# Kernel tuning notes

Measured on AMD Instinct MI355X. Metric: run time of the kernel, lower is better.

Reference implementation:

```python
import jax, jax.numpy as jnp
import numpy as np

H = 512          # hidden_dim
D = 128          # input_dim
L = 8            # output_dim == NUMLABELS
T = 64           # encoder time steps per frame-feature sequence
W = 240          # WINDOWWIDTH (encoder batch dim, one element per frame)
CTX = W // 4     # 60 attention positions
NSTEPS = W // 8


def _lstm(x, Wih, Whh, bih, bhh):
    """PyTorch-convention LSTM (gate order i,f,g,o). x: (T,B,Din) -> (outputs (T,B,H), final h (B,H))."""
    B = x.shape[1]
    Hh = Whh.shape[1]
    xp = jnp.einsum('tbd,gd->tbg', x, Wih) + bih + bhh  # fold both biases
    def step(carry, g):
        h, c = carry
        g = g + h @ Whh.T
        i, f, gg, o = jnp.split(g, 4, axis=-1)
        c = jax.nn.sigmoid(f) * c + jax.nn.sigmoid(i) * jnp.tanh(gg)
        h = jax.nn.sigmoid(o) * jnp.tanh(c)
        return (h, c), h
    z = jnp.zeros((B, Hh), x.dtype)
    (hT, _), hs = jax.lax.scan(step, (z, z), xp)
    return hs, hT


def _forward(data, enc_Wih, enc_Whh, enc_bih, enc_bhh,
             p1f_Wih, p1f_Whh, p1f_bih, p1f_bhh, p1b_Wih, p1b_Whh, p1b_bih, p1b_bhh,
             p2f_Wih, p2f_Whh, p2f_bih, p2f_bhh, p2b_Wih, p2b_Whh, p2b_bih, p2b_bhh,
             attn_W, attn_b, comb_W, comb_b,
             gru_Wih, gru_Whh, gru_bih, gru_bhh, out_W, out_b):
    # --- encoder: per-frame LSTM over T steps, keep final hidden per frame ---
    _, h_enc = _lstm(data, enc_Wih, enc_Whh, enc_bih, enc_bhh)          # (W, H)
    # --- pyramidal bi-LSTM 1: pairs of frames ---
    x1 = h_enc.reshape(W // 2, 1, 2 * H)
    f1, _ = _lstm(x1, p1f_Wih, p1f_Whh, p1f_bih, p1f_bhh)
    b1, _ = _lstm(x1[::-1], p1b_Wih, p1b_Whh, p1b_bih, p1b_bhh)
    # --- pyramidal bi-LSTM 2 ---
    x2 = jnp.concatenate([f1, b1[::-1]], axis=-1).reshape(W // 4, 1, 4 * H)
    f2, h2T = _lstm(x2, p2f_Wih, p2f_Whh, p2f_bih, p2f_bhh)
    b2, _ = _lstm(x2[::-1], p2b_Wih, p2b_Whh, p2b_bih, p2b_bhh)
    ctx = jnp.concatenate([f2, b2[::-1]], axis=-1).reshape(CTX, 2 * H)  # (60, 2H)
    h = h2T[0]                                   # forward-direction final hidden, (H,)
    inp0 = jnp.zeros((L,), data.dtype).at[L - 1].set(1.0)  # one_hot(NOLABEL)

    def dec_step(carry, _):
        inp, h = carry
        aw = jax.nn.softmax(attn_W @ jnp.concatenate([inp, h]) + attn_b)    # (60,)
        applied = aw @ ctx                                                   # (2H,)
        o = jax.nn.relu(comb_W @ jnp.concatenate([inp, applied]) + comb_b)  # (H,)
        # PyTorch GRU cell (gate order r,z,n)
        gi = gru_Wih @ o + gru_bih
        gh = gru_Whh @ h + gru_bhh
        ir, iz, inn = jnp.split(gi, 3)
        hr, hz, hn = jnp.split(gh, 3)
        r = jax.nn.sigmoid(ir + hr)
        z = jax.nn.sigmoid(iz + hz)
        n = jnp.tanh(inn + r * hn)
        h_new = (1.0 - z) * n + z * h
        logp = jax.nn.log_softmax(out_W @ h_new + out_b)                     # (L,)
        return (logp, h_new), logp  # prediction feeds back as next input (y=None path)

    _, outputs = jax.lax.scan(dec_step, (inp0, h), None, length=NSTEPS)
    return outputs  # (30, L)


def setup_inputs() -> dict:
    key = jax.random.key(0)
    ks = iter(jax.random.split(key, 64))
    def mk(*shape):
        return (jax.random.normal(next(ks), shape) * 0.05).astype(jnp.float32)
    d = {"data": jax.random.normal(next(ks), (T, W, D), dtype=jnp.float32)}
    d.update(enc_Wih=mk(4 * H, D), enc_Whh=mk(4 * H, H), enc_bih=mk(4 * H), enc_bhh=mk(4 * H))
    for p, din in (("p1f", 2 * H), ("p1b", 2 * H), ("p2f", 4 * H), ("p2b", 4 * H)):
        d[p + "_Wih"] = mk(4 * H, din)
        d[p + "_Whh"] = mk(4 * H, H)
        d[p + "_bih"] = mk(4 * H)
        d[p + "_bhh"] = mk(4 * H)
    d.update(attn_W=mk(CTX, H + L), attn_b=mk(CTX), comb_W=mk(H, 2 * H + L), comb_b=mk(H),
             gru_Wih=mk(3 * H, H), gru_Whh=mk(3 * H, H), gru_bih=mk(3 * H), gru_bhh=mk(3 * H),
             out_W=mk(L, H), out_b=mk(L))
    return d


def reference(data, enc_Wih, enc_Whh, enc_bih, enc_bhh,
              p1f_Wih, p1f_Whh, p1f_bih, p1f_bhh, p1b_Wih, p1b_Whh, p1b_bih, p1b_bhh,
              p2f_Wih, p2f_Whh, p2f_bih, p2f_bhh, p2b_Wih, p2b_Whh, p2b_bih, p2b_bhh,
              attn_W, attn_b, comb_W, comb_b,
              gru_Wih, gru_Whh, gru_bih, gru_bhh, out_W, out_b):
    return _forward(data, enc_Wih, enc_Whh, enc_bih, enc_bhh,
                    p1f_Wih, p1f_Whh, p1f_bih, p1f_bhh, p1b_Wih, p1b_Whh, p1b_bih, p1b_bhh,
                    p2f_Wih, p2f_Whh, p2f_bih, p2f_bhh, p2b_Wih, p2b_Whh, p2b_bih, p2b_bhh,
                    attn_W, attn_b, comb_W, comb_b,
                    gru_Wih, gru_Whh, gru_bih, gru_bhh, out_W, out_b)
```

## Files before the change

kernel.cpp:

```cpp
#include <hip/hip_runtime.h>
#include <math.h>


typedef __attribute__((ext_vector_type(8))) short short8;
typedef __attribute__((ext_vector_type(4))) float floatx4;
typedef unsigned long long ull;

__device__ __forceinline__ float sigf(float x) { return 1.f / (1.f + __expf(-x)); }
__device__ __forceinline__ float tanh_f(float x) {
    float e = __expf(2.f * x);
    return 1.f - 2.f / (e + 1.f);
}
__device__ __forceinline__ unsigned short f2b(float x) {
    unsigned u = __float_as_uint(x);
    unsigned r = (u + 0x7FFFu + ((u >> 16) & 1u)) >> 16;
    return (unsigned short)r;
}

__device__ __forceinline__ float gld(const float* p) {
    return __hip_atomic_load(p, __ATOMIC_RELAXED, __HIP_MEMORY_SCOPE_AGENT);
}
__device__ __forceinline__ void gst(float* p, float v) {
    __hip_atomic_store(p, v, __ATOMIC_RELAXED, __HIP_MEMORY_SCOPE_AGENT);
}
__device__ __forceinline__ ull gldll(const ull* p) {
    return __hip_atomic_load(p, __ATOMIC_RELAXED, __HIP_MEMORY_SCOPE_AGENT);
}
__device__ __forceinline__ void gstll(ull* p, ull v) {
    __hip_atomic_store(p, v, __ATOMIC_RELAXED, __HIP_MEMORY_SCOPE_AGENT);
}
__device__ __forceinline__ ull packfe(float d, int ep) {
    return ((ull)(unsigned)ep << 32) | (ull)__float_as_uint(d);
}
__device__ __forceinline__ float lowf(ull v) { return __uint_as_float((unsigned)v); }

__global__ void init_k(float* __restrict__ ws) {
    for (int i = blockIdx.x * blockDim.x + threadIdx.x; i < 256000; i += gridDim.x * blockDim.x)
        ws[i] = 0.f;
}

__global__ void __launch_bounds__(256, 1) enc_all(
    const float* __restrict__ data,
    const float* __restrict__ Wih, const float* __restrict__ Whh,
    const float* __restrict__ bih, const float* __restrict__ bhh,
    ull* __restrict__ hbufF,
    float* __restrict__ henc)
{
    __shared__ short act2[20 * 64 * 8];
    __shared__ float gw[4][640];
    __shared__ float cs[512];
    __shared__ short hw[4][16][8];
    __shared__ float biasL[4][4][8];

    const int tid = threadIdx.x;
    const int fg = blockIdx.x >> 4, ds = blockIdx.x & 15;
    const int w = tid >> 6, lane = tid & 63;
    const int n = lane & 15, q = lane >> 4;

    short8 bfrag[2][20];
#pragma unroll
    for (int nt = 0; nt < 2; ++nt) {
        int rr = nt * 16 + n;
        int g = rr >> 3, dp = rr & 7;
        int grow = g * 512 + ds * 32 + w * 8 + dp;
#pragma unroll
        for (int kt = 0; kt < 20; ++kt) {
            int k0 = kt * 32 + q * 8;
            const float* src = (k0 < 512) ? (Whh + (size_t)grow * 512 + k0)
                                          : (Wih + (size_t)grow * 128 + (k0 - 512));
            float4 lo = *(const float4*)src;
            float4 hi = *(const float4*)(src + 4);
            short8 bf;
            bf[0] = (short)f2b(lo.x); bf[1] = (short)f2b(lo.y);
            bf[2] = (short)f2b(lo.z); bf[3] = (short)f2b(lo.w);
            bf[4] = (short)f2b(hi.x); bf[5] = (short)f2b(hi.y);
            bf[6] = (short)f2b(hi.z); bf[7] = (short)f2b(hi.w);
            bfrag[nt][kt] = bf;
        }
    }
    if (tid < 128) {
        int w2 = tid >> 5, rr = tid & 31;
        int g = rr >> 3, dp = rr & 7;
        int grow = g * 512 + ds * 32 + w2 * 8 + dp;
        biasL[w2][g][dp] = bih[grow] + bhh[grow];
    }
    for (int i = tid; i < 512; i += 256) cs[i] = 0.f;
    __syncthreads();

    unsigned* a2u = (unsigned*)act2;

    for (int t = 0; t < 64; ++t) {
        const int kt2 = tid >> 6, l2 = tid & 63, f2v = l2 & 15, q2 = l2 >> 4;
        const float* xs = data + ((size_t)t * 240 + fg * 16 + f2v) * 128 + kt2 * 32 + q2 * 8;
        float4 lo = *(const float4*)xs;
        float4 hi = *(const float4*)(xs + 4);

        {
            const ull* hsrc = hbufF + (size_t)((t & 1) * 15 + fg) * 4096;
            ull v[16];
            for (;;) {
                bool ok = true;
#pragma unroll
                for (int k2 = 0; k2 < 16; ++k2) {
                    v[k2] = gldll(hsrc + tid + 256 * k2);
                    ok &= ((int)(v[k2] >> 32) == t);
                }
                if (ok) break;
                __builtin_amdgcn_s_sleep(1);
            }
#pragma unroll
            for (int k2 = 0; k2 < 16; ++k2)
                a2u[tid + 256 * k2] = (unsigned)v[k2];
        }
        {
            short8 xp;
            xp[0] = (short)f2b(lo.x); xp[1] = (short)f2b(lo.y);
            xp[2] = (short)f2b(lo.z); xp[3] = (short)f2b(lo.w);
            xp[4] = (short)f2b(hi.x); xp[5] = (short)f2b(hi.y);
            xp[6] = (short)f2b(hi.z); xp[7] = (short)f2b(hi.w);
            *(short8*)&act2[((16 + kt2) * 64 + l2) * 8] = xp;
        }
        __syncthreads();

        floatx4 acc0 = {0.f, 0.f, 0.f, 0.f};
        floatx4 acc1 = {0.f, 0.f, 0.f, 0.f};
#pragma unroll
        for (int kt = 0; kt < 20; ++kt) {
            short8 a = *(short8*)&act2[(kt * 64 + lane) * 8];
            acc0 = __builtin_amdgcn_mfma_f32_16x16x32_bf16(a, bfrag[0][kt], acc0, 0, 0, 0);
            acc1 = __builtin_amdgcn_mfma_f32_16x16x32_bf16(a, bfrag[1][kt], acc1, 0, 0, 0);
        }
        *(floatx4*)&gw[w][(0 * 16 + n) * 20 + 4 * q] = acc0;
        *(floatx4*)&gw[w][(1 * 16 + n) * 20 + 4 * q] = acc1;

        int nb = (t + 1) & 1;
#pragma unroll
        for (int it = 0; it < 2; ++it) {
            int f = lane & 15, dp = q + 4 * it;
            float gi = gw[w][(0 * 8 + dp) * 20 + f] + biasL[w][0][dp];
            float gf = gw[w][(1 * 8 + dp) * 20 + f] + biasL[w][1][dp];
            float gg = gw[w][(2 * 8 + dp) * 20 + f] + biasL[w][2][dp];
            float go = gw[w][(3 * 8 + dp) * 20 + f] + biasL[w][3][dp];
            int ci = f * 32 + w * 8 + dp;
            float cc = cs[ci];
            float cn = sigf(gf) * cc + sigf(gi) * tanh_f(gg);
            float hn = sigf(go) * tanh_f(cn);
            cs[ci] = cn;
            hw[w][f][dp] = (short)f2b(hn);
            if (t == 63)
                gst(&henc[(size_t)(fg * 16 + f) * 512 + ds * 32 + w * 8 + dp], hn);
        }
        if (lane < 16) {
            const unsigned* hwu = (const unsigned*)&hw[w][lane][0];
            ull* dst = hbufF + (size_t)(nb * 15 + fg) * 4096 + (ds * 64 + w * 16 + lane) * 4;
            const ull ep = ((ull)(unsigned)(t + 1)) << 32;
#pragma unroll
            for (int r = 0; r < 4; ++r)
                gstll(dst + r, ep | (ull)hwu[r]);
        }
        __syncthreads();
    }
}

__global__ void __launch_bounds__(256) gemm_xp2(
    const float* __restrict__ A, int M, int K, int halfgrid,
    const float* __restrict__ WvF, const float* __restrict__ baF,
    const float* __restrict__ bbF, float* __restrict__ CF,
    const float* __restrict__ WvB, const float* __restrict__ baB,
    const float* __restrict__ bbB, float* __restrict__ CB)
{
    __shared__ float At[16][66];
    __shared__ float Wt[128][66];
    const int tid = threadIdx.x;
    int bgl = blockIdx.x;
    const int rev = (bgl >= halfgrid) ? 1 : 0;
    if (rev) bgl -= halfgrid;
    const float* Wv = rev ? WvB : WvF;
    const float* ba = rev ? baB : baF;
    const float* bb = rev ? bbB : bbF;
    float* C        = rev ? CB : CF;

    const int nt = bgl & 15, mt = bgl >> 4;
    const int rp = tid >> 2, fq = tid & 3;
    const int lr0 = 2 * rp, lr1 = lr0 + 1;
    const int n0 = nt * 128 + lr0, n1 = n0 + 1;

    float acc0[4], acc1[4];
    {
        float b0 = ba[n0] + bb[n0], b1 = ba[n1] + bb[n1];
#pragma unroll
        for (int j = 0; j < 4; ++j) { acc0[j] = b0; acc1[j] = b1; }
    }

    for (int kt = 0; kt < K; kt += 64) {
        {
            int f = tid >> 4, c4 = tid & 15;
            int m = mt * 16 + f;
            float4 v = make_float4(0.f, 0.f, 0.f, 0.f);
            if (m < M) {
                int ar = rev ? (M - 1 - m) : m;
                v = ((const float4*)(A + (size_t)ar * K + kt))[c4];
            }
            At[f][c4 * 4 + 0] = v.x; At[f][c4 * 4 + 1] = v.y;
            At[f][c4 * 4 + 2] = v.z; At[f][c4 * 4 + 3] = v.w;
        }
        for (int i = tid; i < 2048; i += 256) {
            int lr = i >> 4, c4 = i & 15;
            float4 v = ((const float4*)(Wv + (size_t)(nt * 128 + lr) * K + kt))[c4];
            Wt[lr][c4 * 4 + 0] = v.x; Wt[lr][c4 * 4 + 1] = v.y;
            Wt[lr][c4 * 4 + 2] = v.z; Wt[lr][c4 * 4 + 3] = v.w;
        }
        __syncthreads();
        const float2* w0p = (const float2*)(&Wt[lr0][0]);
        const float2* w1p = (const float2*)(&Wt[lr1][0]);
#pragma unroll 8
        for (int kh = 0; kh < 32; ++kh) {
            float2 w0 = w0p[kh], w1 = w1p[kh];
#pragma unroll
            for (int j = 0; j < 4; ++j) {
                float2 av = ((const float2*)(&At[4 * fq + j][0]))[kh];
                acc0[j] += w0.x * av.x + w0.y * av.y;
                acc1[j] += w1.x * av.x + w1.y * av.y;
            }
        }
        __syncthreads();
    }
#pragma unroll
    for (int j = 0; j < 4; ++j) {
        int m = mt * 16 + 4 * fq + j;
        if (m < M) {
            C[(size_t)m * 2048 + n0] = acc0[j];
            C[(size_t)m * 2048 + n1] = acc1[j];
        }
    }
}

__global__ void __launch_bounds__(256, 1) pyr_rec(
    const float* __restrict__ xpF, const float* __restrict__ xpB,
    const float* __restrict__ WhhF, const float* __restrict__ WhhB,
    ull* __restrict__ hp,
    float* __restrict__ outF, float* __restrict__ outB,
    int steps)
{
    const int tid = threadIdx.x;
    const int dir = blockIdx.x >> 6, blk = blockIdx.x & 63;
    const float* xp  = dir ? xpB : xpF;
    const float* Whh = dir ? WhhB : WhhF;
    float* outp = dir ? outB : outF;
    ull* hpd = hp + (size_t)dir * 1024;

    __shared__ __align__(16) float hcur[512];
    __shared__ float red[32][9];
    __shared__ float gv[32];

    const int lr = tid & 31, seg = tid >> 5;
    const int grow = (lr >> 3) * 512 + blk * 8 + (lr & 7);
    float4 wl4[16];
#pragma unroll
    for (int j = 0; j < 16; ++j)
        wl4[j] = *(const float4*)&Whh[(size_t)grow * 512 + 4 * seg + 32 * j];

    const int growx = (tid >> 3) * 512 + blk * 8 + (tid & 7);
    float creg = 0.f;
    __syncthreads();

    for (int t = 0; t < steps; ++t) {
        float xg = 0.f;
        if (tid < 32) xg = xp[(size_t)t * 2048 + growx];
        {
            const ull* base = hpd + (size_t)(t & 1) * 512;
            ull v0 = gldll(base + tid), v1 = gldll(base + tid + 256);
            while (((int)(v0 >> 32) != t) | ((int)(v1 >> 32) != t)) {
                __builtin_amdgcn_s_sleep(1);
                v0 = gldll(base + tid);
                v1 = gldll(base + tid + 256);
            }
            hcur[tid]       = lowf(v0);
            hcur[tid + 256] = lowf(v1);
        }
        __syncthreads();

        float a = 0.f;
#pragma unroll
        for (int j = 0; j < 16; ++j) {
            float4 w = wl4[j];
            float4 h4 = *(const float4*)&hcur[4 * seg + 32 * j];
            a += w.x*h4.x + w.y*h4.y + w.z*h4.z + w.w*h4.w;
        }
        red[lr][seg] = a;
        __syncthreads();

        if (tid < 32) {
            float g = xg;
#pragma unroll
            for (int s2 = 0; s2 < 8; ++s2) g += red[tid][s2];
            gv[tid] = g;
        }
        __syncthreads();
        if (tid < 8) {
            float i_ = sigf(gv[tid]), f_ = sigf(gv[8 + tid]);
            float g_ = tanh_f(gv[16 + tid]), o_ = sigf(gv[24 + tid]);
            creg = f_ * creg + i_ * g_;
            float hn = o_ * tanh_f(creg);
            int d = blk * 8 + tid;
            gstll(&hpd[((t + 1) & 1) * 512 + d], packfe(hn, t + 1));
            int row = dir ? (steps - 1 - t) : t;
            outp[(size_t)row * 512 + d] = hn;
        }
        __syncthreads();
    }
}

__global__ void x2_assemble(const float* __restrict__ f1, const float* __restrict__ b1o,
                            float* __restrict__ x2)
{
    int j = blockIdx.x;
    for (int k = threadIdx.x; k < 2048; k += 256) {
        int q = k >> 9, r = k & 511;
        const float* src = (q & 1) ? b1o : f1;
        int row = 2 * j + (q >> 1);
        x2[(size_t)j * 2048 + k] = src[(size_t)row * 512 + r];
    }
}

__global__ void ctx_k(const float* __restrict__ f2, const float* __restrict__ b2o,
                      float* __restrict__ ctx, ull* __restrict__ hdec_p)
{
    int j = blockIdx.x;
    for (int k = threadIdx.x; k < 1024; k += 256)
        ctx[(size_t)j * 1024 + k] = (k < 512) ? f2[(size_t)j * 512 + k]
                                              : b2o[(size_t)j * 512 + k - 512];
    if (j == 0) {
        for (int i = threadIdx.x; i < 512; i += 256)
            hdec_p[i] = packfe(f2[59 * 512 + i], 0);
    }
}

__global__ void __launch_bounds__(256) precomp_M(
    const float* __restrict__ comb_W,
    const float* __restrict__ ctx,
    float* __restrict__ Mg)
{
    __shared__ float cw[8 * 1024];
    const int tid = threadIdx.x, d0 = blockIdx.x * 8;
    for (int i = tid; i < 2048; i += 256) {
        int r = i >> 8, c4 = i & 255;
        float4 v = *(const float4*)&comb_W[(size_t)(d0 + r) * 1032 + 8 + 4 * c4];
        *(float4*)&cw[r * 1024 + 4 * c4] = v;
    }
    __syncthreads();
    for (int o = tid; o < 480; o += 256) {
        int dl = o / 60, j = o % 60;
        const float4* cp = (const float4*)&cw[dl * 1024];
        const float4* xp = (const float4*)(ctx + (size_t)j * 1024);
        float a = 0.f;
#pragma unroll 4
        for (int k = 0; k < 256; ++k) {
            float4 w = cp[k], x = xp[k];
            a += w.x * x.x + w.y * x.y + w.z * x.z + w.w * x.w;
        }
        Mg[(size_t)(d0 + dl) * 60 + j] = a;
    }
}

__global__ void __launch_bounds__(256, 1) dec_k(
    const float* __restrict__ attn_W, const float* __restrict__ attn_b,
    const float* __restrict__ comb_W, const float* __restrict__ comb_b,
    const float* __restrict__ gWih, const float* __restrict__ gWhh,
    const float* __restrict__ gbih, const float* __restrict__ gbhh,
    const float* __restrict__ outW, const float* __restrict__ outb,
    const float* __restrict__ Mg,
    ull* __restrict__ hdec_p,
    float* __restrict__ dout)
{
    const int tid = threadIdx.x, bid = blockIdx.x;
    const int dbase = bid * 8;

    __shared__ float M2[512][70];
    __shared__ __align__(16) float hx[528];
    __shared__ __align__(16) float xl[512];
    __shared__ __align__(8) float awx[68];
    __shared__ float redA[64][5];
    __shared__ float redGH[32][9];
    __shared__ float redG[32][9];
    __shared__ float redO[8][33];
    __shared__ float biasg[24], biasi[24];
    __shared__ float cbL[512];
    __shared__ float attnbL[64];

    float4 wa4[33], wo4[4], wg4[16], wi4[16];
    const int rz = tid >> 2, sz = tid & 3;
    const int ro = tid >> 5, so = tid & 31;
    const int rg = tid >> 3, sg = tid & 7;

    {
        int rr = (rz < 60) ? rz : 59;
#pragma unroll
        for (int i = 0; i < 32; ++i)
            wa4[i] = *(const float4*)&attn_W[(size_t)rr * 520 + 4 * sz + 16 * i];
        float* wap = (float*)&wa4[32];
#pragma unroll
        for (int r = 0; r < 4; ++r) {
            int k = 4 * sz + 512 + r;
            wap[r] = (k < 520) ? attn_W[(size_t)rr * 520 + k] : 0.f;
        }
    }
#pragma unroll
    for (int i = 0; i < 4; ++i)
        wo4[i] = *(const float4*)&outW[(size_t)ro * 512 + 4 * so + 128 * i];
    {
        int rr = (rg < 24) ? rg : 23;
        int grow = (rr >> 3) * 512 + dbase + (rr & 7);
#pragma unroll
        for (int j = 0; j < 16; ++j) {
            wg4[j] = *(const float4*)&gWhh[(size_t)grow * 512 + 4 * sg + 32 * j];
            wi4[j] = *(const float4*)&gWih[(size_t)grow * 512 + 4 * sg + 32 * j];
        }
    }
    if (tid < 24) {
        int g2 = (tid >> 3) * 512 + dbase + (tid & 7);
        biasg[tid] = gbhh[g2];
        biasi[tid] = gbih[g2];
    }
    for (int i = tid; i < 512; i += 256) cbL[i] = comb_b[i];
    if (tid < 64) attnbL[tid] = (tid < 60) ? attn_b[tid] : 0.f;
    if (tid < 8) hx[520 + tid] = 0.f;
    for (int i = tid; i < 512 * 15; i += 256) {
        int r = i / 15, c4 = i % 15;
        float4 v = *(const float4*)&Mg[(size_t)r * 60 + 4 * c4];
        M2[r][4 * c4 + 0] = v.x; M2[r][4 * c4 + 1] = v.y;
        M2[r][4 * c4 + 2] = v.z; M2[r][4 * c4 + 3] = v.w;
    }
    for (int i = tid; i < 512 * 2; i += 256) {
        int r = i >> 1, h4 = i & 1;
        float4 v = *(const float4*)&comb_W[(size_t)r * 1032 + 4 * h4];
        M2[r][60 + 4 * h4 + 0] = v.x; M2[r][60 + 4 * h4 + 1] = v.y;
        M2[r][60 + 4 * h4 + 2] = v.z; M2[r][60 + 4 * h4 + 3] = v.w;
    }
    __syncthreads();

    for (int s = 0; s < 30; ++s) {
        {
            const ull* hs = hdec_p + (size_t)(s & 1) * 512;
            ull v0 = gldll(hs + tid), v1 = gldll(hs + tid + 256);
            while (((int)(v0 >> 32) != s) | ((int)(v1 >> 32) != s)) {
                __builtin_amdgcn_s_sleep(1);
                v0 = gldll(hs + tid);
                v1 = gldll(hs + tid + 256);
            }
            hx[8 + tid]       = lowf(v0);
            hx[8 + tid + 256] = lowf(v1);
        }
        __syncthreads();

        if (s > 0) {
            float a = 0.f;
#pragma unroll
            for (int i = 0; i < 4; ++i) {
                float4 w = wo4[i];
                float4 h4 = *(const float4*)&hx[8 + 4 * so + 128 * i];
                a += w.x*h4.x + w.y*h4.y + w.z*h4.z + w.w*h4.w;
            }
            redO[ro][so] = a;
        }
        {
            float a = 0.f;
#pragma unroll
            for (int j = 0; j < 16; ++j) {
                float4 w = wg4[j];
                float4 h4 = *(const float4*)&hx[8 + 4 * sg + 32 * j];
                a += w.x*h4.x + w.y*h4.y + w.z*h4.z + w.w*h4.w;
            }
            redGH[rg][sg] = a;
        }
        __syncthreads();

        if (tid < 8) {
            float v;
            if (s > 0) {
                float a = outb[tid];
#pragma unroll
                for (int g2 = 0; g2 < 32; ++g2) a += redO[tid][g2];
                float m = a;
                m = fmaxf(m, __shfl_xor(m, 1));
                m = fmaxf(m, __shfl_xor(m, 2));
                m = fmaxf(m, __shfl_xor(m, 4));
                float e = __expf(a - m);
                float ss2 = e;
                ss2 += __shfl_xor(ss2, 1);
                ss2 += __shfl_xor(ss2, 2);
                ss2 += __shfl_xor(ss2, 4);
                v = a - m - __logf(ss2);
                if (bid == 0) dout[(s - 1) * 8 + tid] = v;
            } else {
                v = (tid == 7) ? 1.f : 0.f;
            }
            hx[tid] = v;
            awx[60 + tid] = v;
        }
        __syncthreads();

        {
            float a = 0.f;
#pragma unroll
            for (int i = 0; i < 33; ++i) {
                float4 w = wa4[i];
                float4 x4 = *(const float4*)&hx[4 * sz + 16 * i];
                a += w.x*x4.x + w.y*x4.y + w.z*x4.z + w.w*x4.w;
            }
            redA[rz][sz] = a;
        }
        __syncthreads();

        if (tid < 64) {
            float z = -1e30f;
            if (tid < 60)
                z = attnbL[tid] + redA[tid][0] + redA[tid][1] + redA[tid][2] + redA[tid][3];
            float m = z;
#pragma unroll
            for (int off = 32; off; off >>= 1) m = fmaxf(m, __shfl_xor(m, off));
            float e = (tid < 60) ? __expf(z - m) : 0.f;
            float ss2 = e;
#pragma unroll
            for (int off = 32; off; off >>= 1) ss2 += __shfl_xor(ss2, off);
            if (tid < 60) awx[tid] = e / ss2;
        }
        __syncthreads();

#pragma unroll
        for (int half = 0; half < 2; ++half) {
            int c = tid + half * 256;
            float a = cbL[c];
            const float2* mrow = (const float2*)&M2[c][0];
            const float2* xv = (const float2*)&awx[0];
#pragma unroll
            for (int jj = 0; jj < 34; ++jj) {
                float2 mm = mrow[jj], xx = xv[jj];
                a += mm.x * xx.x + mm.y * xx.y;
            }
            xl[c] = fmaxf(a, 0.f);
        }
        __syncthreads();

        {
            float a = 0.f;
#pragma unroll
            for (int j = 0; j < 16; ++j) {
                float4 w = wi4[j];
                float4 o4 = *(const float4*)&xl[4 * sg + 32 * j];
                a += w.x*o4.x + w.y*o4.y + w.z*o4.z + w.w*o4.w;
            }
            redG[rg][sg] = a;
        }
        __syncthreads();

        if (tid < 8) {
            float gh0 = biasg[tid], gh1 = biasg[8 + tid], gh2 = biasg[16 + tid];
            float gi0 = biasi[tid], gi1 = biasi[8 + tid], gi2 = biasi[16 + tid];
#pragma unroll
            for (int g2 = 0; g2 < 8; ++g2) {
                gh0 += redGH[tid][g2]; gh1 += redGH[8 + tid][g2]; gh2 += redGH[16 + tid][g2];
                gi0 += redG[tid][g2];  gi1 += redG[8 + tid][g2];  gi2 += redG[16 + tid][g2];
            }
            float r_ = sigf(gi0 + gh0);
            float z_ = sigf(gi1 + gh1);
            float n_ = tanh_f(gi2 + r_ * gh2);
            float hnew = (1.f - z_) * n_ + z_ * hx[8 + dbase + tid];
            gstll(&hdec_p[(size_t)((s + 1) & 1) * 512 + dbase + tid], packfe(hnew, s + 1));
        }
        __syncthreads();
    }

    if (bid == 0) {
        {
            const ull* hs = hdec_p + (size_t)(30 & 1) * 512;
            ull v0 = gldll(hs + tid), v1 = gldll(hs + tid + 256);
            while (((int)(v0 >> 32) != 30) | ((int)(v1 >> 32) != 30)) {
                __builtin_amdgcn_s_sleep(1);
                v0 = gldll(hs + tid);
                v1 = gldll(hs + tid + 256);
            }
            hx[8 + tid]       = lowf(v0);
            hx[8 + tid + 256] = lowf(v1);
        }
        __syncthreads();
        {
            float a = 0.f;
#pragma unroll
            for (int i = 0; i < 4; ++i) {
                float4 w = wo4[i];
                float4 h4 = *(const float4*)&hx[8 + 4 * so + 128 * i];
                a += w.x*h4.x + w.y*h4.y + w.z*h4.z + w.w*h4.w;
            }
            redO[ro][so] = a;
        }
        __syncthreads();
        if (tid < 8) {
            float a = outb[tid];
#pragma unroll
            for (int g2 = 0; g2 < 32; ++g2) a += redO[tid][g2];
            float m = a;
            m = fmaxf(m, __shfl_xor(m, 1));
            m = fmaxf(m, __shfl_xor(m, 2));
            m = fmaxf(m, __shfl_xor(m, 4));
            float e = __expf(a - m);
            float ss2 = e;
            ss2 += __shfl_xor(ss2, 1);
            ss2 += __shfl_xor(ss2, 2);
            ss2 += __shfl_xor(ss2, 4);
            dout[29 * 8 + tid] = a - m - __logf(ss2);
        }
    }
}

extern "C" void kernel_launch(void* const* d_in, const int* in_sizes, int n_in,
                              void* d_out, int out_size, void* d_ws, size_t ws_size,
                              hipStream_t stream) {
    (void)in_sizes; (void)n_in; (void)out_size; (void)ws_size;
    const float* data    = (const float*)d_in[0];
    const float* enc_Wih = (const float*)d_in[1];
    const float* enc_Whh = (const float*)d_in[2];
    const float* enc_bih = (const float*)d_in[3];
    const float* enc_bhh = (const float*)d_in[4];
    const float* p1f_Wih = (const float*)d_in[5];
    const float* p1f_Whh = (const float*)d_in[6];
    const float* p1f_bih = (const float*)d_in[7];
    const float* p1f_bhh = (const float*)d_in[8];
    const float* p1b_Wih = (const float*)d_in[9];
    const float* p1b_Whh = (const float*)d_in[10];
    const float* p1b_bih = (const float*)d_in[11];
    const float* p1b_bhh = (const float*)d_in[12];
    const float* p2f_Wih = (const float*)d_in[13];
    const float* p2f_Whh = (const float*)d_in[14];
    const float* p2f_bih = (const float*)d_in[15];
    const float* p2f_bhh = (const float*)d_in[16];
    const float* p2b_Wih = (const float*)d_in[17];
    const float* p2b_Whh = (const float*)d_in[18];
    const float* p2b_bih = (const float*)d_in[19];
    const float* p2b_bhh = (const float*)d_in[20];
    const float* attn_W  = (const float*)d_in[21];
    const float* attn_b  = (const float*)d_in[22];
    const float* comb_W  = (const float*)d_in[23];
    const float* comb_b  = (const float*)d_in[24];
    const float* gru_Wih = (const float*)d_in[25];
    const float* gru_Whh = (const float*)d_in[26];
    const float* gru_bih = (const float*)d_in[27];
    const float* gru_bhh = (const float*)d_in[28];
    const float* out_W   = (const float*)d_in[29];
    const float* out_b   = (const float*)d_in[30];

    float* ws = (float*)d_ws;
    ull* hbufF   = (ull*)ws;
    ull* hp1     = (ull*)(ws + 245760);
    ull* hp2     = (ull*)(ws + 249856);
    ull* hdec_p  = (ull*)(ws + 253952);
    float* henc  = ws + 256000;
    float* xp1f  = ws + 378880;
    float* xp1b  = ws + 624640;
    float* f1    = ws + 870400;
    float* b1o   = ws + 931840;
    float* x2    = ws + 993280;
    float* xp2f  = ws + 1116160;
    float* xp2b  = ws + 1239040;
    float* f2    = ws + 1361920;
    float* b2o   = ws + 1392640;
    float* ctxb  = ws + 1423360;
    float* Mg    = ws + 1484800;

    init_k<<<256, 256, 0, stream>>>(ws);

    enc_all<<<240, 256, 0, stream>>>(data, enc_Wih, enc_Whh, enc_bih, enc_bhh,
                                     hbufF, henc);
    gemm_xp2<<<256, 256, 0, stream>>>(henc, 120, 1024, 128,
                                      p1f_Wih, p1f_bih, p1f_bhh, xp1f,
                                      p1b_Wih, p1b_bih, p1b_bhh, xp1b);
    pyr_rec<<<128, 256, 0, stream>>>(xp1f, xp1b, p1f_Whh, p1b_Whh, hp1, f1, b1o, 120);
    x2_assemble<<<60, 256, 0, stream>>>(f1, b1o, x2);
    gemm_xp2<<<128, 256, 0, stream>>>(x2, 60, 2048, 64,
                                      p2f_Wih, p2f_bih, p2f_bhh, xp2f,
                                      p2b_Wih, p2b_bih, p2b_bhh, xp2b);
    pyr_rec<<<128, 256, 0, stream>>>(xp2f, xp2b, p2f_Whh, p2b_Whh, hp2, f2, b2o, 60);
    ctx_k<<<60, 256, 0, stream>>>(f2, b2o, ctxb, hdec_p);
    precomp_M<<<64, 256, 0, stream>>>(comb_W, ctxb, Mg);
    dec_k<<<64, 256, 0, stream>>>(attn_W, attn_b, comb_W, comb_b,
                                  gru_Wih, gru_Whh, gru_bih, gru_bhh,
                                  out_W, out_b, Mg, hdec_p,
                                  (float*)d_out);
}
```

Baseline: 1.318 ms.

## Restructure decoder kernel to 512 threads with shuffle reductions and fewer barriers

The decoder kernel moves from 256 to 512 threads per block and swaps its shared-memory partial-sum arrays for wave shuffle reductions. The attention logits are split into a hidden-state part, computed in parallel with the GRU hidden and output projections, and an 8-wide label part folded into the softmax wave. This removes two block barriers per decode step and shortens the serial chain on the recurrent critical path. The cost is more threads per block and different register pressure, and the decoder is only part of the total pipeline time.

```diff
diff --git a/kernel.cpp b/kernel.cpp
--- a/kernel.cpp
+++ b/kernel.cpp
@@ -363,7 +363,7 @@
     }
 }
 
-__global__ void __launch_bounds__(256, 1) dec_k(
+__global__ void __launch_bounds__(512, 1) dec_k(
     const float* __restrict__ attn_W, const float* __restrict__ attn_b,
     const float* __restrict__ comb_W, const float* __restrict__ comb_b,
     const float* __restrict__ gWih, const float* __restrict__ gWhh,
@@ -374,64 +374,67 @@
     float* __restrict__ dout)
 {
     const int tid = threadIdx.x, bid = blockIdx.x;
+    const int lane = tid & 63, wv = tid >> 6;
     const int dbase = bid * 8;
 
     __shared__ float M2[512][70];
-    __shared__ __align__(16) float hx[528];
+    __shared__ __align__(16) float hL[520];
     __shared__ __align__(16) float xl[512];
-    __shared__ __align__(8) float awx[68];
-    __shared__ float redA[64][5];
-    __shared__ float redGH[32][9];
-    __shared__ float redG[32][9];
-    __shared__ float redO[8][33];
+    __shared__ __align__(16) float awx[68];
+    __shared__ float zd[8], zh[64];
+    __shared__ float ghl[24], gil[24];
     __shared__ float biasg[24], biasi[24];
     __shared__ float cbL[512];
-    __shared__ float attnbL[64];
-
-    float4 wa4[33], wo4[4], wg4[16], wi4[16];
-    const int rz = tid >> 2, sz = tid & 3;
-    const int ro = tid >> 5, so = tid & 31;
-    const int rg = tid >> 3, sg = tid & 7;
-
+    __shared__ float attnbL[64], outbL[8];
+
+    const int rg = tid >> 4, sg = tid & 15;
+    const int rz = tid >> 3, szz = tid & 7;
+
+    float4 wo2[2];
+    float4 wg8[8], wi8[8];
+    float4 wzh[16];
+    float4 wip[2];
+    {
+        const float* wp = outW + (size_t)wv * 512 + lane * 8;
+        wo2[0] = *(const float4*)wp;
+        wo2[1] = *(const float4*)(wp + 4);
+    }
+    {
+        int rr = (rg < 24) ? rg : 23;
+        size_t grow = (size_t)((rr >> 3) * 512 + dbase + (rr & 7)) * 512 + sg * 32;
+#pragma unroll
+        for (int i = 0; i < 8; ++i) {
+            wg8[i] = *(const float4*)&gWhh[grow + 4 * i];
+            wi8[i] = *(const float4*)&gWih[grow + 4 * i];
+        }
+    }
     {
         int rr = (rz < 60) ? rz : 59;
-#pragma unroll
-        for (int i = 0; i < 32; ++i)
-            wa4[i] = *(const float4*)&attn_W[(size_t)rr * 520 + 4 * sz + 16 * i];
-        float* wap = (float*)&wa4[32];
-#pragma unroll
-        for (int r = 0; r < 4; ++r) {
-            int k = 4 * sz + 512 + r;
-            wap[r] = (k < 520) ? attn_W[(size_t)rr * 520 + k] : 0.f;
-        }
-    }
-#pragma unroll
-    for (int i = 0; i < 4; ++i)
-        wo4[i] = *(const float4*)&outW[(size_t)ro * 512 + 4 * so + 128 * i];
+        size_t base = (size_t)rr * 520 + 8 + szz * 64;
+#pragma unroll
+        for (int i = 0; i < 16; ++i)
+            wzh[i] = *(const float4*)&attn_W[base + 4 * i];
+    }
     {
-        int rr = (rg < 24) ? rg : 23;
-        int grow = (rr >> 3) * 512 + dbase + (rr & 7);
-#pragma unroll
-        for (int j = 0; j < 16; ++j) {
-            wg4[j] = *(const float4*)&gWhh[(size_t)grow * 512 + 4 * sg + 32 * j];
-            wi4[j] = *(const float4*)&gWih[(size_t)grow * 512 + 4 * sg + 32 * j];
-        }
+        int rr = (tid < 60) ? tid : 59;
+        wip[0] = *(const float4*)&attn_W[(size_t)rr * 520 + 0];
+        wip[1] = *(const float4*)&attn_W[(size_t)rr * 520 + 4];
     }
     if (tid < 24) {
         int g2 = (tid >> 3) * 512 + dbase + (tid & 7);
         biasg[tid] = gbhh[g2];
         biasi[tid] = gbih[g2];
     }
-    for (int i = tid; i < 512; i += 256) cbL[i] = comb_b[i];
+    if (tid < 512) cbL[tid] = comb_b[tid];
     if (tid < 64) attnbL[tid] = (tid < 60) ? attn_b[tid] : 0.f;
-    if (tid < 8) hx[520 + tid] = 0.f;
-    for (int i = tid; i < 512 * 15; i += 256) {
+    if (tid < 8) outbL[tid] = outb[tid];
+    for (int i = tid; i < 512 * 15; i += 512) {
         int r = i / 15, c4 = i % 15;
         float4 v = *(const float4*)&Mg[(size_t)r * 60 + 4 * c4];
         M2[r][4 * c4 + 0] = v.x; M2[r][4 * c4 + 1] = v.y;
         M2[r][4 * c4 + 2] = v.z; M2[r][4 * c4 + 3] = v.w;
     }
-    for (int i = tid; i < 512 * 2; i += 256) {
+    for (int i = tid; i < 512 * 2; i += 512) {
         int r = i >> 1, h4 = i & 1;
         float4 v = *(const float4*)&comb_W[(size_t)r * 1032 + 4 * h4];
         M2[r][60 + 4 * h4 + 0] = v.x; M2[r][60 + 4 * h4 + 1] = v.y;
@@ -442,130 +445,131 @@
     for (int s = 0; s < 30; ++s) {
         {
             const ull* hs = hdec_p + (size_t)(s & 1) * 512;
-            ull v0 = gldll(hs + tid), v1 = gldll(hs + tid + 256);
-            while (((int)(v0 >> 32) != s) | ((int)(v1 >> 32) != s)) {
+            ull v0 = gldll(hs + tid);
+            while ((int)(v0 >> 32) != s) {
                 __builtin_amdgcn_s_sleep(1);
                 v0 = gldll(hs + tid);
-                v1 = gldll(hs + tid + 256);
-            }
-            hx[8 + tid]       = lowf(v0);
-            hx[8 + tid + 256] = lowf(v1);
-        }
-        __syncthreads();
-
-        if (s > 0) {
+            }
+            hL[tid] = lowf(v0);
+        }
+        __syncthreads();
+
+        {
             float a = 0.f;
-#pragma unroll
-            for (int i = 0; i < 4; ++i) {
-                float4 w = wo4[i];
-                float4 h4 = *(const float4*)&hx[8 + 4 * so + 128 * i];
+            const float4* h4p = (const float4*)&hL[lane * 8];
+            float4 h0 = h4p[0], h1 = h4p[1];
+            a += wo2[0].x*h0.x + wo2[0].y*h0.y + wo2[0].z*h0.z + wo2[0].w*h0.w;
+            a += wo2[1].x*h1.x + wo2[1].y*h1.y + wo2[1].z*h1.z + wo2[1].w*h1.w;
+#pragma unroll
+            for (int off = 32; off; off >>= 1) a += __shfl_xor(a, off);
+            if (lane == 0) zd[wv] = a;
+        }
+        {
+            float a = 0.f;
+            const float* hb = &hL[sg * 32];
+#pragma unroll
+            for (int i = 0; i < 8; ++i) {
+                float4 w = wg8[i];
+                float4 h4 = *(const float4*)&hb[4 * i];
                 a += w.x*h4.x + w.y*h4.y + w.z*h4.z + w.w*h4.w;
             }
-            redO[ro][so] = a;
+            a += __shfl_xor(a, 1); a += __shfl_xor(a, 2);
+            a += __shfl_xor(a, 4); a += __shfl_xor(a, 8);
+            if (sg == 0 && rg < 24) ghl[rg] = a;
         }
         {
             float a = 0.f;
-#pragma unroll
-            for (int j = 0; j < 16; ++j) {
-                float4 w = wg4[j];
-                float4 h4 = *(const float4*)&hx[8 + 4 * sg + 32 * j];
+            const float* hb = &hL[szz * 64];
+#pragma unroll
+            for (int i = 0; i < 16; ++i) {
+                float4 w = wzh[i];
+                float4 h4 = *(const float4*)&hb[4 * i];
                 a += w.x*h4.x + w.y*h4.y + w.z*h4.z + w.w*h4.w;
             }
-            redGH[rg][sg] = a;
-        }
-        __syncthreads();
-
-        if (tid < 8) {
-            float v;
-            if (s > 0) {
-                float a = outb[tid];
-#pragma unroll
-                for (int g2 = 0; g2 < 32; ++g2) a += redO[tid][g2];
-                float m = a;
-                m = fmaxf(m, __shfl_xor(m, 1));
-                m = fmaxf(m, __shfl_xor(m, 2));
-                m = fmaxf(m, __shfl_xor(m, 4));
-                float e = __expf(a - m);
-                float ss2 = e;
-                ss2 += __shfl_xor(ss2, 1);
-                ss2 += __shfl_xor(ss2, 2);
-                ss2 += __shfl_xor(ss2, 4);
-                v = a - m - __logf(ss2);
-                if (bid == 0) dout[(s - 1) * 8 + tid] = v;
-            } else {
-                v = (tid == 7) ? 1.f : 0.f;
-            }
-            hx[tid] = v;
-            awx[60 + tid] = v;
-        }
-        __syncthreads();
-
-        {
-            float a = 0.f;
-#pragma unroll
-            for (int i = 0; i < 33; ++i) {
-                float4 w = wa4[i];
-                float4 x4 = *(const float4*)&hx[4 * sz + 16 * i];
-                a += w.x*x4.x + w.y*x4.y + w.z*x4.z + w.w*x4.w;
-            }
-            redA[rz][sz] = a;
-        }
-        __syncthreads();
-
-        if (tid < 64) {
+            a += __shfl_xor(a, 1); a += __shfl_xor(a, 2); a += __shfl_xor(a, 4);
+            if (szz == 0 && rz < 60) zh[rz] = a;
+        }
+        __syncthreads();
+
+        if (wv == 0) {
+            if (lane < 8) {
+                float v;
+                if (s > 0) {
+                    float a = zd[lane] + outbL[lane];
+                    float m = a;
+                    m = fmaxf(m, __shfl_xor(m, 1));
+                    m = fmaxf(m, __shfl_xor(m, 2));
+                    m = fmaxf(m, __shfl_xor(m, 4));
+                    float e = __expf(a - m);
+                    float ss2 = e;
+                    ss2 += __shfl_xor(ss2, 1);
+                    ss2 += __shfl_xor(ss2, 2);
+                    ss2 += __shfl_xor(ss2, 4);
+                    v = a - m - __logf(ss2);
+                    if (bid == 0) dout[(s - 1) * 8 + lane] = v;
+                } else {
+                    v = (lane == 7) ? 1.f : 0.f;
+                }
+                awx[60 + lane] = v;
+            }
             float z = -1e30f;
-            if (tid < 60)
-                z = attnbL[tid] + redA[tid][0] + redA[tid][1] + redA[tid][2] + redA[tid][3];
+            if (lane < 60) {
+                z = zh[lane] + attnbL[lane]
+                  + wip[0].x * awx[60] + wip[0].y * awx[61]
+                  + wip[0].z * awx[62] + wip[0].w * awx[63]
+                  + wip[1].x * awx[64] + wip[1].y * awx[65]
+                  + wip[1].z * awx[66] + wip[1].w * awx[67];
+            }
             float m = z;
 #pragma unroll
             for (int off = 32; off; off >>= 1) m = fmaxf(m, __shfl_xor(m, off));
-            float e = (tid < 60) ? __expf(z - m) : 0.f;
+            float e = (lane < 60) ? __expf(z - m) : 0.f;
             float ss2 = e;
 #pragma unroll
             for (int off = 32; off; off >>= 1) ss2 += __shfl_xor(ss2, off);
-            if (tid < 60) awx[tid] = e / ss2;
-        }
-        __syncthreads();
-
-#pragma unroll
-        for (int half = 0; half < 2; ++half) {
-            int c = tid + half * 256;
-            float a = cbL[c];
-            const float2* mrow = (const float2*)&M2[c][0];
+            if (lane < 60) awx[lane] = e / ss2;
+        }
+        __syncthreads();
+
+        {
+            float a = cbL[tid];
+            const float2* mrow = (const float2*)&M2[tid][0];
             const float2* xv = (const float2*)&awx[0];
 #pragma unroll
             for (int jj = 0; jj < 34; ++jj) {
                 float2 mm = mrow[jj], xx = xv[jj];
                 a += mm.x * xx.x + mm.y * xx.y;
             }
-            xl[c] = fmaxf(a, 0.f);
+            xl[tid] = fmaxf(a, 0.f);
         }
         __syncthreads();
 
         {
             float a = 0.f;
-#pragma unroll
-            for (int j = 0; j < 16; ++j) {
-                float4 w = wi4[j];
-                float4 o4 = *(const float4*)&xl[4 * sg + 32 * j];
+            const float* ob = &xl[sg * 32];
+#pragma unroll
+            for (int i = 0; i < 8; ++i) {
+                float4 w = wi8[i];
+                float4 o4 = *(const float4*)&ob[4 * i];
                 a += w.x*o4.x + w.y*o4.y + w.z*o4.z + w.w*o4.w;
             }
-            redG[rg][sg] = a;
+            a += __shfl_xor(a, 1); a += __shfl_xor(a, 2);
+            a += __shfl_xor(a, 4); a += __shfl_xor(a, 8);
+            if (sg == 0 && rg < 24) gil[rg] = a;
         }
         __syncthreads();
 
         if (tid < 8) {
-            float gh0 = biasg[tid], gh1 = biasg[8 + tid], gh2 = biasg[16 + tid];
-            float gi0 = biasi[tid], gi1 = biasi[8 + tid], gi2 = biasi[16 + tid];
-#pragma unroll
-            for (int g2 = 0; g2 < 8; ++g2) {
-                gh0 += redGH[tid][g2]; gh1 += redGH[8 + tid][g2]; gh2 += redGH[16 + tid][g2];
-                gi0 += redG[tid][g2];  gi1 += redG[8 + tid][g2];  gi2 += redG[16 + tid][g2];
-            }
+            float gh0 = biasg[tid] + ghl[tid];
+            float gh1 = biasg[8 + tid] + ghl[8 + tid];
+            float gh2 = biasg[16 + tid] + ghl[16 + tid];
+            float gi0 = biasi[tid] + gil[tid];
+            float gi1 = biasi[8 + tid] + gil[8 + tid];
+            float gi2 = biasi[16 + tid] + gil[16 + tid];
             float r_ = sigf(gi0 + gh0);
             float z_ = sigf(gi1 + gh1);
             float n_ = tanh_f(gi2 + r_ * gh2);
-            float hnew = (1.f - z_) * n_ + z_ * hx[8 + dbase + tid];
+            float hnew = (1.f - z_) * n_ + z_ * hL[dbase + tid];
             gstll(&hdec_p[(size_t)((s + 1) & 1) * 512 + dbase + tid], packfe(hnew, s + 1));
         }
         __syncthreads();
@@ -574,31 +578,27 @@
     if (bid == 0) {
         {
             const ull* hs = hdec_p + (size_t)(30 & 1) * 512;
-            ull v0 = gldll(hs + tid), v1 = gldll(hs + tid + 256);
-            while (((int)(v0 >> 32) != 30) | ((int)(v1 >> 32) != 30)) {
+            ull v0 = gldll(hs + tid);
+            while ((int)(v0 >> 32) != 30) {
                 __builtin_amdgcn_s_sleep(1);
                 v0 = gldll(hs + tid);
-                v1 = gldll(hs + tid + 256);
-            }
-            hx[8 + tid]       = lowf(v0);
-            hx[8 + tid + 256] = lowf(v1);
+            }
+            hL[tid] = lowf(v0);
         }
         __syncthreads();
         {
             float a = 0.f;
-#pragma unroll
-            for (int i = 0; i < 4; ++i) {
-                float4 w = wo4[i];
-                float4 h4 = *(const float4*)&hx[8 + 4 * so + 128 * i];
-                a += w.x*h4.x + w.y*h4.y + w.z*h4.z + w.w*h4.w;
-            }
-            redO[ro][so] = a;
+            const float4* h4p = (const float4*)&hL[lane * 8];
+            float4 h0 = h4p[0], h1 = h4p[1];
+            a += wo2[0].x*h0.x + wo2[0].y*h0.y + wo2[0].z*h0.z + wo2[0].w*h0.w;
+            a += wo2[1].x*h1.x + wo2[1].y*h1.y + wo2[1].z*h1.z + wo2[1].w*h1.w;
+#pragma unroll
+            for (int off = 32; off; off >>= 1) a += __shfl_xor(a, off);
+            if (lane == 0) zd[wv] = a;
         }
         __syncthreads();
         if (tid < 8) {
-            float a = outb[tid];
-#pragma unroll
-            for (int g2 = 0; g2 < 32; ++g2) a += redO[tid][g2];
+            float a = zd[tid] + outbL[tid];
             float m = a;
             m = fmaxf(m, __shfl_xor(m, 1));
             m = fmaxf(m, __shfl_xor(m, 2));
@@ -682,7 +682,7 @@
     pyr_rec<<<128, 256, 0, stream>>>(xp2f, xp2b, p2f_Whh, p2b_Whh, hp2, f2, b2o, 60);
     ctx_k<<<60, 256, 0, stream>>>(f2, b2o, ctxb, hdec_p);
     precomp_M<<<64, 256, 0, stream>>>(comb_W, ctxb, Mg);
-    dec_k<<<64, 256, 0, stream>>>(attn_W, attn_b, comb_W, comb_b,
+    dec_k<<<64, 512, 0, stream>>>(attn_W, attn_b, comb_W, comb_b,
                                   gru_Wih, gru_Whh, gru_bih, gru_bhh,
                                   out_W, out_b, Mg, hdec_p,
                                   (float*)d_out);
```

Measured after the change: 1.291 ms. 1.02x faster.
